# Kernel optimization log

Hardware: AMD Instinct MI355X
Metric: run time of the kernel (lower is better)

## Reference

```python
import jax, jax.numpy as jnp
import numpy as np

B, N, K = 32, 64, 128          # batch, atoms per cell, channel width (128x0e + 128x1o)
R_MAX = 5.0
NUM_BESSEL = 8
P_CUT = 5                       # num_polynomial_cutoff
AVG_NEIGH = 16.0                # avg_num_neighbors
H_MLP = 512                     # hidden_dimensions_size, n_hidden_dimensions = 2
FEAT = 5 * K                    # ((num_interactions-1)*4 + 1) * 128 = 640


def silu(x):
    return x * jax.nn.sigmoid(x)


def _bessel_cutoff(r, mask):
    # Bessel radial basis * polynomial cutoff (MACE), masked on valid edges.
    n = jnp.arange(1, NUM_BESSEL + 1, dtype=r.dtype)
    rb = jnp.sqrt(2.0 / R_MAX) * jnp.sin(n * (jnp.pi / R_MAX) * r[..., None]) / r[..., None]
    u = r / R_MAX
    p = float(P_CUT)
    fc = 1.0 - 0.5 * (p + 1) * (p + 2) * u**P_CUT + p * (p + 2) * u**(P_CUT + 1) - 0.5 * p * (p + 1) * u**(P_CUT + 2)
    fc = fc * (u < 1.0)
    return rb * (fc * mask)[..., None]


def _sph(uvec):
    # Real spherical harmonics l=0,1,2 (component normalization), uvec: unit edge vectors.
    x, y, z = uvec[..., 0], uvec[..., 1], uvec[..., 2]
    s3, s5, s15 = 3.0**0.5, 5.0**0.5, 15.0**0.5
    Y0 = jnp.ones_like(x)[..., None]
    Y1 = jnp.stack([s3 * x, s3 * y, s3 * z], -1)
    Y2 = jnp.stack([s15 * x * y, s15 * y * z, 0.5 * s5 * (3 * z * z - 1.0),
                    s15 * x * z, 0.5 * s15 * (x * x - y * y)], -1)
    return Y0, Y1, Y2


def _radial_mlp(x, w0, b0, w1, b1, w2, b2, w3, b3):
    h = silu(x @ w0 + b0)
    h = silu(h @ w1 + b1)
    h = silu(h @ w2 + b2)
    return h @ w3 + b3


def setup_inputs() -> dict:
    key = jax.random.key(0)
    ks = jax.random.split(key, 32)
    f32 = jnp.float32

    def lin(k, fan_in, shape):
        return (jax.random.normal(k, shape, dtype=f32) / np.sqrt(fan_in)).astype(f32)

    inp = {
        "noisy_relative_positions": jax.random.uniform(ks[0], (B, N, 3), dtype=f32),
        "time": jax.random.uniform(ks[1], (B, 1), dtype=f32),
        "unit_cell": (11.0 * jnp.eye(3, dtype=f32) + 0.3 * jax.random.uniform(ks[2], (B, 3, 3), dtype=f32)),
        "w_embed": lin(ks[3], 1, (K,)),
        # interaction 1 radial MLP: 8 -> 64 -> 64 -> 64 -> 3*K (weights for l=0,1,2 paths)
        "r1_w0": lin(ks[4], NUM_BESSEL, (NUM_BESSEL, 64)), "r1_b0": jnp.zeros((64,), f32),
        "r1_w1": lin(ks[5], 64, (64, 64)), "r1_b1": jnp.zeros((64,), f32),
        "r1_w2": lin(ks[6], 64, (64, 64)), "r1_b2": jnp.zeros((64,), f32),
        "r1_w3": lin(ks[7], 64, (64, 3 * K)), "r1_b3": jnp.zeros((3 * K,), f32),
        "mix1_l0": lin(ks[8], K, (K, K)),
        "mix1_l1": lin(ks[9], K, (K, K)),
        "mix1_l2": lin(ks[10], K, (K, K)),
        # interaction 2 radial MLP: 8 -> 64 -> 64 -> 64 -> 2*K (paths 0e x 0e -> 0e, 1o x 1o -> 0e)
        "r2_w0": lin(ks[11], NUM_BESSEL, (NUM_BESSEL, 64)), "r2_b0": jnp.zeros((64,), f32),
        "r2_w1": lin(ks[12], 64, (64, 64)), "r2_b1": jnp.zeros((64,), f32),
        "r2_w2": lin(ks[13], 64, (64, 64)), "r2_b2": jnp.zeros((64,), f32),
        "r2_w3": lin(ks[14], 64, (64, 2 * K)), "r2_b3": jnp.zeros((2 * K,), f32),
        "mix2": lin(ks[15], K, (K, K)),
        # readout MLP: 641 -> 512 -> 512 -> 3
        "mlp_w0": lin(ks[16], FEAT + 1, (FEAT + 1, H_MLP)), "mlp_b0": jnp.zeros((H_MLP,), f32),
        "mlp_w1": lin(ks[17], H_MLP, (H_MLP, H_MLP)), "mlp_b1": jnp.zeros((H_MLP,), f32),
        "mlp_w2": lin(ks[18], H_MLP, (H_MLP, 3)), "mlp_b2": jnp.zeros((3,), f32),
    }
    return inp


def reference(noisy_relative_positions, time, unit_cell, w_embed,
              r1_w0, r1_b0, r1_w1, r1_b1, r1_w2, r1_b2, r1_w3, r1_b3,
              mix1_l0, mix1_l1, mix1_l2,
              r2_w0, r2_b0, r2_w1, r2_b1, r2_w2, r2_b2, r2_w3, r2_b3, mix2,
              mlp_w0, mlp_b0, mlp_w1, mlp_b1, mlp_w2, mlp_b2):
    frac = noisy_relative_positions                      # [B,N,3] fractional
    d = frac[:, :, None, :] - frac[:, None, :, :]        # [B,N,N,3]
    d = d - jnp.round(d)                                 # minimum-image PBC
    dc = jnp.einsum('bijc,bcd->bijd', d, unit_cell)      # cartesian displacements
    r = jnp.sqrt(jnp.maximum(jnp.sum(dc * dc, -1), 1e-12))
    mask = (r < R_MAX) & (~jnp.eye(N, dtype=bool))[None]
    r_safe = jnp.where(mask, r, 1.0)
    uvec = dc / r_safe[..., None] * mask[..., None]      # unit edge vectors (0 off-edge)

    rad = _bessel_cutoff(r_safe, mask)                   # [B,N,N,8]
    Y0, Y1, Y2 = _sph(uvec)                              # [B,N,N,1|3|5]

    h0 = jnp.broadcast_to(w_embed, (B, N, K))            # element embedding (single species)

    # ---- interaction 1: radial-weighted tensor product h_j (x) Y_l, scatter over j ----
    we = _radial_mlp(rad, r1_w0, r1_b0, r1_w1, r1_b1, r1_w2, r1_b2, r1_w3, r1_b3)
    we = we.reshape(B, N, N, 3, K) * mask[..., None, None]
    hj = h0[:, None, :, :]                               # sender features [B,1,N,K]
    msg0 = jnp.einsum('bijk,bijm->bimk', we[..., 0, :] * hj, Y0)[:, :, 0] / AVG_NEIGH  # [B,N,K]
    msg1 = jnp.einsum('bijk,bijm->bimk', we[..., 1, :] * hj, Y1) / AVG_NEIGH           # [B,N,3,K]
    msg2 = jnp.einsum('bijk,bijm->bimk', we[..., 2, :] * hj, Y2) / AVG_NEIGH           # [B,N,5,K]

    s1 = msg0 @ mix1_l0 + jnp.sum(msg2 * msg2, axis=2) @ mix1_l2   # scalars [B,N,K]
    v1 = jnp.einsum('bimk,kc->bimc', msg1, mix1_l1)                # vectors [B,N,3,K]
    h1 = silu(s1)

    # ---- interaction 2: scalar output from 0e x 0e and 1o x 1o -> 0e paths ----
    we2 = _radial_mlp(rad, r2_w0, r2_b0, r2_w1, r2_b1, r2_w2, r2_b2, r2_w3, r2_b3)
    we2 = we2.reshape(B, N, N, 2, K) * mask[..., None, None]
    msg_a = jnp.sum(we2[..., 0, :] * h1[:, None, :, :], axis=2)    # [B,N,K]
    inv = jnp.einsum('bijm,bjmk->bijk', Y1, v1)                    # Y1 . v1_j invariant
    msg_b = jnp.sum(we2[..., 1, :] * inv, axis=2)
    s2 = ((msg_a + msg_b) / AVG_NEIGH) @ mix2                      # [B,N,K]

    # node_feats: layer1 full irreps (128x0e + 128x1o -> 512) + layer2 scalars (128) = 640
    node_feats = jnp.concatenate([s1, v1.reshape(B, N, 3 * K), s2], axis=-1)

    t = jnp.broadcast_to(time[:, None, :], (B, N, 1))
    x = jnp.concatenate([node_feats, t], axis=-1)                  # [B,N,641]
    x = jax.nn.relu(x @ mlp_w0 + mlp_b0)
    x = jax.nn.relu(x @ mlp_w1 + mlp_b1)
    return x @ mlp_w2 + mlp_b2                                     # [B,N,3]
```

## Files before the change

### kernel.cpp

```cpp
#include <hip/hip_runtime.h>
#include <math.h>

#define B_ 32
#define N_ 64
#define K_ 128
#define NPAIR (B_*N_*N_)
#define NTRI 2080
#define GEOM_BLOCKS 260
#define PREP_COUNT 741376
#define PREP_BLOCKS 2896

typedef __attribute__((ext_vector_type(8))) short short8;
typedef __attribute__((ext_vector_type(8))) __bf16 bf16x8;
typedef __attribute__((ext_vector_type(4))) float floatx4;

__device__ __forceinline__ float silu_f(float x) {
    float e = __builtin_amdgcn_exp2f(-1.442695040888963f * x);
    return x * __builtin_amdgcn_rcpf(1.0f + e);
}
__device__ __forceinline__ float4 ld4(const float* p) { return *(const float4*)p; }

__device__ __forceinline__ short f2bf(float x) {
    union { float f; unsigned u; } v; v.f = x;
    unsigned r = (v.u + 0x7FFFu + ((v.u >> 16) & 1u)) >> 16;
    return (short)r;
}
__device__ __forceinline__ float bf2f(short s) {
    union { unsigned u; float f; } v;
    v.u = ((unsigned)(unsigned short)s) << 16;
    return v.f;
}
__device__ __forceinline__ bf16x8 ld_frag(const short* p) {
    short8 r = *(const short8*)p;
    return __builtin_bit_cast(bf16x8, r);
}

__device__ __forceinline__ int2 tri_decode(int t) {
    float f = (129.0f - sqrtf((float)(16641 - 8*t))) * 0.5f;
    int i = (int)f;
    int off = 64*i - (i*(i-1))/2;
    if (off > t) { i--; off = 64*i - (i*(i-1))/2; }
    else {
        int offn = 64*(i+1) - ((i+1)*i)/2;
        if (offn <= t) { i = i+1; off = offn; }
    }
    return make_int2(i, i + (t - off));
}

__global__ __launch_bounds__(256) void pre_kernel(
    const float* __restrict__ pos, const float* __restrict__ cell,
    short* __restrict__ radbf, float* __restrict__ Y1, float* __restrict__ Y2,
    float* __restrict__ maskf,
    const float* __restrict__ r1w0, const float* __restrict__ r1w1,
    const float* __restrict__ r1w2, const float* __restrict__ r1w3,
    const float* __restrict__ r2w0, const float* __restrict__ r2w1,
    const float* __restrict__ r2w2, const float* __restrict__ r2w3,
    const float* __restrict__ r2b3,
    const float* __restrict__ mw0, const float* __restrict__ mw1,
    const float* __restrict__ wemb,
    const float* __restrict__ l0, const float* __restrict__ l1,
    const float* __restrict__ l2, short* __restrict__ dst)
{
    int t = threadIdx.x;
    if (blockIdx.x < GEOM_BLOCKS) {
        int gt = blockIdx.x * 256 + t;
        int b = gt / NTRI;
        int tt = gt - b*NTRI;
        int2 ij = tri_decode(tt);
        int i = ij.x, j = ij.y;
        const float* pi = pos + (size_t)(b*N_ + i)*3;
        const float* pj = pos + (size_t)(b*N_ + j)*3;
        float d0 = pi[0]-pj[0], d1 = pi[1]-pj[1], d2 = pi[2]-pj[2];
        d0 -= rintf(d0); d1 -= rintf(d1); d2 -= rintf(d2);
        const float* C = cell + b*9;
        float dc0 = d0*C[0] + d1*C[3] + d2*C[6];
        float dc1 = d0*C[1] + d1*C[4] + d2*C[7];
        float dc2 = d0*C[2] + d1*C[5] + d2*C[8];
        float r2 = fmaxf(dc0*dc0 + dc1*dc1 + dc2*dc2, 1e-12f);
        float r = sqrtf(r2);
        bool m = (r < 5.0f) && (i != j);
        float mf = m ? 1.0f : 0.0f;
        float rs = m ? r : 1.0f;
        float inv_rs = __builtin_amdgcn_rcpf(rs);
        inv_rs = inv_rs * (2.0f - rs*inv_rs);
        float x = dc0*inv_rs*mf, y = dc1*inv_rs*mf, z = dc2*inv_rs*mf;
        float u = r * 0.2f;
        float u2 = u*u, u4 = u2*u2, u5 = u4*u;
        float fc = 1.0f - 21.0f*u5 + 35.0f*u5*u - 15.0f*u5*u2;
        fc = (u < 1.0f) ? fc : 0.0f;
        float pref = 0.6324555320336759f * inv_rs * (fc * mf);
        float rev = 0.1f * rs;
        float sw = __builtin_amdgcn_sinf(rev);
        float cw = __builtin_amdgcn_cosf(rev);
        float c2 = 2.0f * cw;
        short8 sv;
        float sp = 0.f, s = sw;
        #pragma unroll
        for (int n = 0; n < 8; n++) {
            sv[n] = f2bf(pref * s);
            float ns = c2*s - sp;
            sp = s; s = ns;
        }
        size_t pu = ((size_t)b*64 + i)*64 + j;
        size_t pl = ((size_t)b*64 + j)*64 + i;
        *(short8*)&radbf[pu*8] = sv;
        const float s3  = 1.7320508075688772f;
        const float s5  = 2.23606797749979f;
        const float s15 = 3.872983346207417f;
        float y1x = s3*x, y1y = s3*y, y1z = s3*z;
        Y1[pu*3+0] = y1x; Y1[pu*3+1] = y1y; Y1[pu*3+2] = y1z;
        Y1[pl*3+0] = -y1x; Y1[pl*3+1] = -y1y; Y1[pl*3+2] = -y1z;
        float q0 = s15*x*y, q1 = s15*y*z, q2 = 0.5f*s5*(3.0f*z*z - 1.0f);
        float q3 = s15*x*z, q4 = 0.5f*s15*(x*x - y*y);
        Y2[pu*5+0]=q0; Y2[pu*5+1]=q1; Y2[pu*5+2]=q2; Y2[pu*5+3]=q3; Y2[pu*5+4]=q4;
        Y2[pl*5+0]=q0; Y2[pl*5+1]=q1; Y2[pl*5+2]=q2; Y2[pl*5+3]=q3; Y2[pl*5+4]=q4;
        maskf[pu] = mf; maskf[pl] = mf;
        return;
    }
    int idx = (blockIdx.x - GEOM_BLOCKS) * 256 + t;
    if (idx >= PREP_COUNT) return;
    short v;
    if (idx < 4096) {
        int n = idx >> 6, k = idx & 63; v = f2bf(r1w1[k*64 + n]);
    } else if (idx < 8192) {
        int i = idx - 4096; int n = i >> 6, k = i & 63; v = f2bf(r1w2[k*64 + n]);
    } else if (idx < 12288) {
        int i = idx - 8192; int n = i >> 6, k = i & 63; v = f2bf(r2w1[k*64 + n]);
    } else if (idx < 16384) {
        int i = idx - 12288; int n = i >> 6, k = i & 63; v = f2bf(r2w2[k*64 + n]);
    } else if (idx < 40960) {
        int i = idx - 16384; int col = i / 96, k = i - col*96;
        v = (k < 64) ? f2bf(r2w3[k*256 + col])
          : (k == 64) ? f2bf(r2b3[col]) : (short)0;
    } else if (idx < 401408) {
        int i = idx - 40960; int n = i / 704, k = i - n*704;
        v = (k < 641) ? f2bf(mw0[(size_t)k*512 + n]) : (short)0;
    } else if (idx < 663552) {
        int i = idx - 401408; int n = i >> 9, k = i & 511;
        v = f2bf(mw1[(size_t)k*512 + n]);
    } else if (idx < 665600) {
        int i = idx - 663552; int n = i >> 5, k = i & 31;
        v = (k < 8) ? f2bf(r1w0[k*64 + n]) : (short)0;
    } else if (idx < 667648) {
        int i = idx - 665600; int n = i >> 5, k = i & 31;
        v = (k < 8) ? f2bf(r2w0[k*64 + n]) : (short)0;
    } else if (idx < 692224) {
        int i = idx - 667648; int col = i >> 6, h = i & 63;
        v = f2bf(r1w3[h*384 + col] * wemb[col & 127] * 0.0625f);
    } else {
        int i = idx - 692224; int n = i / 384, k = i - n*384;
        float f;
        if (k < 128)       f = l0[k*128 + n];
        else if (k < 256)  f = l2[(k-128)*128 + n];
        else               f = l1[(k-256)*128 + n];
        v = f2bf(f);
    }
    dst[idx] = v;
}

__global__ __launch_bounds__(256) void bigmlp_kernel(
    const short* __restrict__ radbf,
    const short* __restrict__ w0T1, const float* __restrict__ b01,
    const short* __restrict__ w1T1, const float* __restrict__ b11,
    const short* __restrict__ w2T1, const float* __restrict__ b21,
    short* __restrict__ hc1,
    const short* __restrict__ w0T2, const float* __restrict__ b02,
    const short* __restrict__ w1T2, const float* __restrict__ b12,
    const short* __restrict__ w2T2, const float* __restrict__ b22,
    short* __restrict__ hc2)
{
    __shared__ short radB[128*40];
    __shared__ short actA[128*72];
    __shared__ short actB[128*72];
    __shared__ int prs[128];
    int t = threadIdx.x;
    int wv = t >> 6, lane = t & 63, qd = lane >> 4, nn = lane & 15;
    int bb = blockIdx.x / 17;
    int chunk = blockIdx.x - bb*17;

    if (t < 128) {
        int tt0 = chunk*128 + t;
        uint4 z = {0,0,0,0};
        uint4 rv = z;
        int pr = -1;
        if (tt0 < NTRI) {
            int2 ij = tri_decode(tt0);
            pr = (ij.x << 8) | ij.y;
            size_t pu = ((size_t)bb*64 + ij.x)*64 + ij.y;
            rv = *(const uint4*)&radbf[pu*8];
        }
        prs[t] = pr;
        *(uint4*)&radB[t*40]      = rv;
        *(uint4*)&radB[t*40 + 8]  = z;
        *(uint4*)&radB[t*40 + 16] = z;
        *(uint4*)&radB[t*40 + 24] = z;
        *(uint4*)&radB[t*40 + 32] = z;
    }
    __syncthreads();

    const short* w0Ts[2] = {w0T1, w0T2};
    const short* w1Ts[2] = {w1T1, w1T2};
    const short* w2Ts[2] = {w2T1, w2T2};
    const float* b0s[2]  = {b01, b02};
    const float* b1s[2]  = {b11, b12};
    const float* b2s[2]  = {b21, b22};
    short* hcs[2] = {hc1, hc2};

    for (int net = 0; net < 2; net++) {
        const short* w0T = w0Ts[net];
        const short* w1T = w1Ts[net];
        const short* w2T = w2Ts[net];
        const float* b0 = b0s[net];
        const float* b1 = b1s[net];
        const float* b2 = b2s[net];
        short* hc = hcs[net];
        #pragma unroll
        for (int ms = 0; ms < 2; ms++) {
            int r0 = wv*32 + ms*16;
            bf16x8 a = ld_frag(&radB[(r0 + nn)*40 + qd*8]);
            #pragma unroll
            for (int tt = 0; tt < 4; tt++) {
                floatx4 acc = (floatx4){0.f,0.f,0.f,0.f};
                bf16x8 bb_ = ld_frag(&w0T[(tt*16 + nn)*32 + qd*8]);
                acc = __builtin_amdgcn_mfma_f32_16x16x32_bf16(a, bb_, acc, 0, 0, 0);
                int col = tt*16 + nn;
                float bv = b0[col];
                #pragma unroll
                for (int i = 0; i < 4; i++)
                    actA[(r0 + qd*4 + i)*72 + col] = f2bf(silu_f(acc[i] + bv));
            }
        }
        __syncthreads();
        #pragma unroll
        for (int ms = 0; ms < 2; ms++) {
            int r0 = wv*32 + ms*16;
            bf16x8 a0 = ld_frag(&actA[(r0 + nn)*72 + qd*8]);
            bf16x8 a1 = ld_frag(&actA[(r0 + nn)*72 + 32 + qd*8]);
            #pragma unroll
            for (int tt = 0; tt < 4; tt++) {
                floatx4 acc = (floatx4){0.f,0.f,0.f,0.f};
                bf16x8 b0f = ld_frag(&w1T[(tt*16 + nn)*64 + qd*8]);
                bf16x8 b1f = ld_frag(&w1T[(tt*16 + nn)*64 + 32 + qd*8]);
                acc = __builtin_amdgcn_mfma_f32_16x16x32_bf16(a0, b0f, acc, 0, 0, 0);
                acc = __builtin_amdgcn_mfma_f32_16x16x32_bf16(a1, b1f, acc, 0, 0, 0);
                int col = tt*16 + nn;
                float bv = b1[col];
                #pragma unroll
                for (int i = 0; i < 4; i++)
                    actB[(r0 + qd*4 + i)*72 + col] = f2bf(silu_f(acc[i] + bv));
            }
        }
        __syncthreads();
        #pragma unroll
        for (int ms = 0; ms < 2; ms++) {
            int r0 = wv*32 + ms*16;
            bf16x8 a0 = ld_frag(&actB[(r0 + nn)*72 + qd*8]);
            bf16x8 a1 = ld_frag(&actB[(r0 + nn)*72 + 32 + qd*8]);
            #pragma unroll
            for (int tt = 0; tt < 4; tt++) {
                floatx4 acc = (floatx4){0.f,0.f,0.f,0.f};
                bf16x8 b0f = ld_frag(&w2T[(tt*16 + nn)*64 + qd*8]);
                bf16x8 b1f = ld_frag(&w2T[(tt*16 + nn)*64 + 32 + qd*8]);
                acc = __builtin_amdgcn_mfma_f32_16x16x32_bf16(a0, b0f, acc, 0, 0, 0);
                acc = __builtin_amdgcn_mfma_f32_16x16x32_bf16(a1, b1f, acc, 0, 0, 0);
                int col = tt*16 + nn;
                float bv = b2[col];
                #pragma unroll
                for (int i = 0; i < 4; i++) {
                    int pr = prs[r0 + qd*4 + i];
                    if (pr >= 0) {
                        short val = f2bf(silu_f(acc[i] + bv));
                        int pi = pr >> 8, pj = pr & 255;
                        size_t base = (size_t)bb*4096;
                        hc[(base + pi*64 + pj)*64 + col] = val;
                        if (pi != pj)
                            hc[(base + pj*64 + pi)*64 + col] = val;
                    }
                }
            }
        }
        __syncthreads();
    }
}

__global__ __launch_bounds__(256) void msg1_kernel(
    const short* __restrict__ hc1, const float* __restrict__ Y1g,
    const float* __restrict__ Y2g, const float* __restrict__ maskg,
    const float* __restrict__ wemb, const float* __restrict__ b3,
    const short* __restrict__ w3T, const short* __restrict__ lT,
    const float* __restrict__ timeg,
    short* __restrict__ h1bf, float* __restrict__ v1g, short* __restrict__ featsb)
{
    __shared__ __align__(16) char pool[19008];
    short* hcT  = (short*)pool;
    short* A2   = (short*)pool;
    short* YmB  = (short*)(pool + 9216);
    short* GB   = (short*)(pool + 11520);
    float* msgF = (float*)(pool + 13824);
    float* qF   = (float*)(pool + 18432);
    float* SY   = (float*)(pool + 18944);

    int t = threadIdx.x;
    int wv = t >> 6, lane = t & 63, qd = lane >> 4, nn = lane & 15;
    int node = blockIdx.x;
    int b = node >> 6;
    size_t pbase = (size_t)node * 64;

    for (int idx = t; idx < 512; idx += 256) {
        int j = idx >> 3, h0 = (idx & 7)*8;
        short8 v = *(const short8*)&hc1[((size_t)node*64 + j)*64 + h0];
        #pragma unroll
        for (int q = 0; q < 8; q++) hcT[(h0 + q)*72 + j] = v[q];
    }
    for (int idx = t; idx < 1152; idx += 256) YmB[idx] = 0;
    __syncthreads();
    if (t < 64) {
        int j = t;
        float mf = maskg[pbase + j];
        YmB[j] = f2bf(mf);
        #pragma unroll
        for (int m = 0; m < 3; m++) YmB[(1+m)*72 + j] = f2bf(Y1g[(pbase+j)*3 + m] * mf);
        #pragma unroll
        for (int m = 0; m < 5; m++) YmB[(4+m)*72 + j] = f2bf(Y2g[(pbase+j)*5 + m] * mf);
    }
    __syncthreads();
    if (t < 16) {
        float acc = 0.f;
        if (t < 9) for (int j = 0; j < 64; j++) acc += bf2f(YmB[t*72 + j]);
        SY[t] = acc;
    }
    {
        floatx4 accG = (floatx4){0.f,0.f,0.f,0.f};
        #pragma unroll
        for (int ks = 0; ks < 64; ks += 32) {
            bf16x8 a = ld_frag(&YmB[nn*72 + ks + qd*8]);
            bf16x8 bfr = ld_frag(&hcT[(wv*16 + nn)*72 + ks + qd*8]);
            accG = __builtin_amdgcn_mfma_f32_16x16x32_bf16(a, bfr, accG, 0, 0, 0);
        }
        #pragma unroll
        for (int i = 0; i < 4; i++)
            GB[(qd*4 + i)*72 + wv*16 + nn] = f2bf(accG[i]);
    }
    __syncthreads();
    {
        bf16x8 a0f = ld_frag(&GB[nn*72 + 0  + qd*8]);
        bf16x8 a1f = ld_frag(&GB[nn*72 + 32 + qd*8]);
        #pragma unroll
        for (int tl = 0; tl < 6; tl++) {
            int col0 = (wv*6 + tl)*16;
            floatx4 acc = (floatx4){0.f,0.f,0.f,0.f};
            bf16x8 b0f = ld_frag(&w3T[(col0 + nn)*64 + 0  + qd*8]);
            bf16x8 b1f = ld_frag(&w3T[(col0 + nn)*64 + 32 + qd*8]);
            acc = __builtin_amdgcn_mfma_f32_16x16x32_bf16(a0f, b0f, acc, 0, 0, 0);
            acc = __builtin_amdgcn_mfma_f32_16x16x32_bf16(a1f, b1f, acc, 0, 0, 0);
            int col = col0 + nn;
            int csec = col >> 7, k = col & 127;
            #pragma unroll
            for (int i = 0; i < 4; i++) {
                int m = qd*4 + i;
                bool valid = (csec == 0) ? (m == 0)
                           : (csec == 1) ? (m >= 1 && m <= 3)
                                         : (m >= 4 && m <= 8);
                if (valid)
                    msgF[m*128 + k] = acc[i] + SY[m]*b3[col]*wemb[k]*0.0625f;
            }
        }
    }
    __syncthreads();
    if (t < 128) {
        float acc = 0.f;
        #pragma unroll
        for (int m = 4; m < 9; m++) { float v = msgF[m*128 + t]; acc += v*v; }
        qF[t] = acc;
    }
    __syncthreads();
    for (int idx = t; idx < 6272; idx += 256) A2[idx] = 0;
    __syncthreads();
    A2[t] = (t < 128) ? f2bf(msgF[t]) : f2bf(qF[t - 128]);
    if (t < 128) {
        #pragma unroll
        for (int m = 1; m <= 3; m++)
            A2[m*392 + 256 + t] = f2bf(msgF[m*128 + t]);
    }
    __syncthreads();
    #pragma unroll
    for (int tt = 0; tt < 2; tt++) {
        int col = (wv*2 + tt)*16 + nn;
        floatx4 acc = (floatx4){0.f,0.f,0.f,0.f};
        #pragma unroll
        for (int ks = 0; ks < 384; ks += 32) {
            bf16x8 a = ld_frag(&A2[nn*392 + ks + qd*8]);
            bf16x8 bfr = ld_frag(&lT[(size_t)col*384 + ks + qd*8]);
            acc = __builtin_amdgcn_mfma_f32_16x16x32_bf16(a, bfr, acc, 0, 0, 0);
        }
        if (qd == 0) {
            float s1 = acc[0];
            featsb[(size_t)node*704 + col] = f2bf(s1);
            h1bf[(size_t)node*128 + col] = f2bf(silu_f(s1));
            #pragma unroll
            for (int i = 1; i < 4; i++) {
                float v = acc[i];
                v1g[(size_t)node*384 + (i-1)*128 + col] = v;
                featsb[(size_t)node*704 + 128 + (i-1)*128 + col] = f2bf(v);
            }
        }
    }
    if (t == 0) featsb[(size_t)node*704 + 640] = f2bf(timeg[b]);
    if (t < 63) featsb[(size_t)node*704 + 641 + t] = 0;
}

__global__ __launch_bounds__(256) void msg2_kernel(
    const short* __restrict__ hc2, const float* __restrict__ Y1g,
    const float* __restrict__ maskg, const short* __restrict__ w3extT,
    const short* __restrict__ h1bf, const float* __restrict__ v1g,
    const float* __restrict__ mix2, short* __restrict__ featsb)
{
    __shared__ __align__(16) char pool[50688];
    short* hc2e  = (short*)pool;
    short* h1B   = (short*)(pool + 14336);
    short* invB  = (short*)(pool + 31744);
    float* Y1s   = (float*)(pool + 49152);
    float* msgab = (float*)(pool + 50176);

    int t = threadIdx.x;
    int wv = t >> 6, lane = t & 63, qd = lane >> 4, nn = lane & 15;
    int node = blockIdx.x;
    int b = node >> 6;
    size_t pbase = (size_t)node * 64;

    if (t < 64) {
        int j = t;
        #pragma unroll
        for (int m = 0; m < 3; m++) Y1s[j*4 + m] = Y1g[(pbase+j)*3 + m];
        float mf = maskg[pbase + j];
        short8 z8 = {0,0,0,0,0,0,0,0};
        *(short8*)&hc2e[j*112 + 64] = z8;
        *(short8*)&hc2e[j*112 + 72] = z8;
        *(short8*)&hc2e[j*112 + 80] = z8;
        *(short8*)&hc2e[j*112 + 88] = z8;
        *(short8*)&hc2e[j*112 + 96] = z8;
        *(short8*)&hc2e[j*112 + 104] = z8;
        hc2e[j*112 + 64] = f2bf(mf);
    }
    for (int idx = t; idx < 512; idx += 256) {
        int j = idx >> 3, h0 = (idx & 7)*8;
        short8 v = *(const short8*)&hc2[((size_t)node*64 + j)*64 + h0];
        float mf = maskg[pbase + j];
        if (mf == 0.f) { short8 z8 = {0,0,0,0,0,0,0,0}; v = z8; }
        *(short8*)&hc2e[j*112 + h0] = v;
    }
    for (int idx = t; idx < 1024; idx += 256) {
        int j = idx >> 4, k0 = (idx & 15)*8;
        *(uint4*)&h1B[j*136 + k0] = *(const uint4*)&h1bf[((size_t)b*64 + j)*128 + k0];
    }
    if (t < 128) msgab[t] = 0.f;
    __syncthreads();
    for (int idx = t; idx < 2048; idx += 256) {
        int j = idx >> 5, kq = (idx & 31)*4;
        const float* vb = &v1g[((size_t)b*64 + j)*384 + kq];
        float4 vx = ld4(vb), vy = ld4(vb + 128), vz = ld4(vb + 256);
        float yx = Y1s[j*4+0], yy = Y1s[j*4+1], yz = Y1s[j*4+2];
        invB[j*136 + kq + 0] = f2bf(yx*vx.x + yy*vy.x + yz*vz.x);
        invB[j*136 + kq + 1] = f2bf(yx*vx.y + yy*vy.y + yz*vz.y);
        invB[j*136 + kq + 2] = f2bf(yx*vx.z + yy*vy.z + yz*vz.z);
        invB[j*136 + kq + 3] = f2bf(yx*vx.w + yy*vy.w + yz*vz.w);
    }
    __syncthreads();
    {
        bf16x8 a0 = ld_frag(&hc2e[(wv*16 + nn)*112 + 0  + qd*8]);
        bf16x8 a1 = ld_frag(&hc2e[(wv*16 + nn)*112 + 32 + qd*8]);
        bf16x8 a2 = ld_frag(&hc2e[(wv*16 + nn)*112 + 64 + qd*8]);
        for (int g = 0; g < 4; g++) {
            #pragma unroll
            for (int tt = 0; tt < 4; tt++) {
                int col0 = g*64 + tt*16;
                floatx4 acc = (floatx4){0.f,0.f,0.f,0.f};
                bf16x8 b0f = ld_frag(&w3extT[(col0 + nn)*96 + 0  + qd*8]);
                bf16x8 b1f = ld_frag(&w3extT[(col0 + nn)*96 + 32 + qd*8]);
                bf16x8 b2f = ld_frag(&w3extT[(col0 + nn)*96 + 64 + qd*8]);
                acc = __builtin_amdgcn_mfma_f32_16x16x32_bf16(a0, b0f, acc, 0, 0, 0);
                acc = __builtin_amdgcn_mfma_f32_16x16x32_bf16(a1, b1f, acc, 0, 0, 0);
                acc = __builtin_amdgcn_mfma_f32_16x16x32_bf16(a2, b2f, acc, 0, 0, 0);
                int col = col0 + nn;
                int k = col & 127;
                const short* src = (col < 128) ? h1B : invB;
                float p = 0.f;
                #pragma unroll
                for (int i = 0; i < 4; i++) {
                    int j = wv*16 + qd*4 + i;
                    p += acc[i] * bf2f(src[j*136 + k]);
                }
                p += __shfl_xor(p, 16);
                p += __shfl_xor(p, 32);
                if (qd == 0) atomicAdd(&msgab[k], p);
            }
        }
    }
    __syncthreads();
    if (t < 128) {
        float acc = 0.f;
        for (int k = 0; k < 128; k++) acc += msgab[k] * mix2[k*128 + t];
        featsb[(size_t)node*704 + 512 + t] = f2bf(acc * 0.0625f);
    }
}

__global__ __launch_bounds__(256) void gemm_part_kernel(
    const short* __restrict__ A, int lda,
    const short* __restrict__ BT, int ldb,
    int ngran, int nsplit, float* __restrict__ Cp)
{
    int t = threadIdx.x;
    int wv = t >> 6, lane = t & 63, qd = lane >> 4, nn = lane & 15;
    int m0 = blockIdx.x * 64, n0 = blockIdx.y * 64, z = blockIdx.z;
    int g0 = (z*ngran)/nsplit, g1 = ((z+1)*ngran)/nsplit;
    floatx4 acc[4];
    #pragma unroll
    for (int tt = 0; tt < 4; tt++) acc[tt] = (floatx4){0.f,0.f,0.f,0.f};
    int row = wv*16 + nn;
    for (int g = g0; g < g1; g++) {
        int k = g*32;
        bf16x8 a = ld_frag(&A[(size_t)(m0 + row)*lda + k + qd*8]);
        #pragma unroll
        for (int tt = 0; tt < 4; tt++) {
            bf16x8 bb = ld_frag(&BT[(size_t)(n0 + tt*16 + nn)*ldb + k + qd*8]);
            acc[tt] = __builtin_amdgcn_mfma_f32_16x16x32_bf16(a, bb, acc[tt], 0, 0, 0);
        }
    }
    float* out = Cp + (size_t)z*2048*512;
    #pragma unroll
    for (int tt = 0; tt < 4; tt++) {
        int n = n0 + tt*16 + nn;
        #pragma unroll
        for (int i = 0; i < 4; i++)
            out[(size_t)(m0 + wv*16 + qd*4 + i)*512 + n] = acc[tt][i];
    }
}

__global__ __launch_bounds__(256) void combine_kernel(
    const float* __restrict__ Cp, const float* __restrict__ bias,
    short* __restrict__ out)
{
    int idx = (blockIdx.x * 256 + threadIdx.x) * 4;
    int n = idx & 511;
    float4 s = ld4(&Cp[idx]);
    #pragma unroll
    for (int z = 1; z < 4; z++) {
        float4 p = ld4(&Cp[(size_t)z*1048576 + idx]);
        s.x += p.x; s.y += p.y; s.z += p.z; s.w += p.w;
    }
    float4 bv = ld4(&bias[n]);
    short4 o;
    o.x = f2bf(fmaxf(s.x + bv.x, 0.f));
    o.y = f2bf(fmaxf(s.y + bv.y, 0.f));
    o.z = f2bf(fmaxf(s.z + bv.z, 0.f));
    o.w = f2bf(fmaxf(s.w + bv.w, 0.f));
    *(short4*)&out[idx] = o;
}

__global__ __launch_bounds__(64) void final3_kernel(
    const short* __restrict__ H, const float* __restrict__ w2,
    const float* __restrict__ b2, float* __restrict__ out)
{
    int node = blockIdx.x, lane = threadIdx.x;
    float a0 = 0.f, a1 = 0.f, a2 = 0.f;
    #pragma unroll
    for (int r = 0; r < 8; r++) {
        int k = r*64 + lane;
        float h = bf2f(H[(size_t)node*512 + k]);
        a0 += h * w2[k*3 + 0];
        a1 += h * w2[k*3 + 1];
        a2 += h * w2[k*3 + 2];
    }
    #pragma unroll
    for (int off = 32; off > 0; off >>= 1) {
        a0 += __shfl_down(a0, off);
        a1 += __shfl_down(a1, off);
        a2 += __shfl_down(a2, off);
    }
    if (lane == 0) {
        out[(size_t)node*3 + 0] = a0 + b2[0];
        out[(size_t)node*3 + 1] = a1 + b2[1];
        out[(size_t)node*3 + 2] = a2 + b2[2];
    }
}

extern "C" void kernel_launch(void* const* d_in, const int* in_sizes, int n_in,
                              void* d_out, int out_size, void* d_ws, size_t ws_size,
                              hipStream_t stream) {
    const float* pos   = (const float*)d_in[0];
    const float* timeg = (const float*)d_in[1];
    const float* cell  = (const float*)d_in[2];
    const float* wemb  = (const float*)d_in[3];
    const float* r1w0  = (const float*)d_in[4];
    const float* r1b0  = (const float*)d_in[5];
    const float* r1w1  = (const float*)d_in[6];
    const float* r1b1  = (const float*)d_in[7];
    const float* r1w2  = (const float*)d_in[8];
    const float* r1b2  = (const float*)d_in[9];
    const float* r1w3  = (const float*)d_in[10];
    const float* r1b3  = (const float*)d_in[11];
    const float* l0    = (const float*)d_in[12];
    const float* l1    = (const float*)d_in[13];
    const float* l2    = (const float*)d_in[14];
    const float* r2w0  = (const float*)d_in[15];
    const float* r2b0  = (const float*)d_in[16];
    const float* r2w1  = (const float*)d_in[17];
    const float* r2b1  = (const float*)d_in[18];
    const float* r2w2  = (const float*)d_in[19];
    const float* r2b2  = (const float*)d_in[20];
    const float* r2w3  = (const float*)d_in[21];
    const float* r2b3  = (const float*)d_in[22];
    const float* mix2  = (const float*)d_in[23];
    const float* mw0   = (const float*)d_in[24];
    const float* mb0   = (const float*)d_in[25];
    const float* mw1   = (const float*)d_in[26];
    const float* mb1   = (const float*)d_in[27];
    const float* mw2   = (const float*)d_in[28];
    const float* mb2   = (const float*)d_in[29];

    float* ws = (float*)d_ws;
    short* radbf  = (short*)ws;
    float* Y1     = ws + 524288;
    float* Y2     = ws + 917504;
    float* maskf  = ws + 1572864;
    float* v1     = ws + 1703936;
    short* featsb = (short*)(ws + 2490368);
    short* prep   = (short*)(ws + 3211264);
    short* hc1    = (short*)(ws + 3590144);
    short* hc2    = (short*)(ws + 7784448);
    short* h1bf   = (short*)(ws + 11978752);

    short* w1T_1  = prep;
    short* w2T_1  = prep + 4096;
    short* w1T_2  = prep + 8192;
    short* w2T_2  = prep + 12288;
    short* w3extT = prep + 16384;
    short* wT0    = prep + 40960;
    short* wT1    = prep + 401408;
    short* w0T_1  = prep + 663552;
    short* w0T_2  = prep + 665600;
    short* w3T_1  = prep + 667648;
    short* lT     = prep + 692224;

    float* Cp   = (float*)hc1;
    short* h0bb = radbf;
    short* h1bb = (short*)Y2;

    pre_kernel<<<GEOM_BLOCKS + PREP_BLOCKS, 256, 0, stream>>>(
        pos, cell, radbf, Y1, Y2, maskf,
        r1w0, r1w1, r1w2, r1w3, r2w0, r2w1, r2w2, r2w3, r2b3,
        mw0, mw1, wemb, l0, l1, l2, prep);
    bigmlp_kernel<<<32*17, 256, 0, stream>>>(radbf,
        w0T_1, r1b0, w1T_1, r1b1, w2T_1, r1b2, hc1,
        w0T_2, r2b0, w1T_2, r2b1, w2T_2, r2b2, hc2);
    msg1_kernel<<<B_*N_, 256, 0, stream>>>(hc1, Y1, Y2, maskf, wemb, r1b3,
        w3T_1, lT, timeg, h1bf, v1, featsb);
    msg2_kernel<<<B_*N_, 256, 0, stream>>>(hc2, Y1, maskf, w3extT, h1bf, v1,
        mix2, featsb);
    {
        dim3 g(32, 8, 4);
        gemm_part_kernel<<<g, 256, 0, stream>>>(featsb, 704, wT0, 704, 22, 4, Cp);
        combine_kernel<<<1024, 256, 0, stream>>>(Cp, mb0, h0bb);
        gemm_part_kernel<<<g, 256, 0, stream>>>(h0bb, 512, wT1, 512, 16, 4, Cp);
        combine_kernel<<<1024, 256, 0, stream>>>(Cp, mb1, h1bb);
    }
    final3_kernel<<<B_*N_, 64, 0, stream>>>(h1bb, mw2, mb2, (float*)d_out);
}
```

Before: 301.2 us.

## Restructure msg2 into two-node blocks, fold mask into MLP, fuse final combine

The mask is now applied inside the radial MLP epilogue, so msg2 no longer needs the extended bias/mask column and the w3 operand shrinks to K=64 with the bias added after the MFMA. msg2 becomes msg2b, which handles two nodes per block with double-buffered Y1/mask staging, loads hc2 fragments straight from global memory, and replaces shared atomics with per-wave partial sums. The last combine kernel is folded into the final 3-output projection, which now reads the fp32 split-K partials directly. The zero-fill passes in msg1 are also trimmed to only the padding regions, removing two barriers. Risks: reading the fp32 partials in the final kernel costs more bandwidth than bf16, and fewer, larger msg2 blocks reduce parallelism.

```diff
diff --git a/kernel.cpp b/kernel.cpp
--- a/kernel.cpp
+++ b/kernel.cpp
@@ -9,6 +9,7 @@
 #define GEOM_BLOCKS 260
 #define PREP_COUNT 741376
 #define PREP_BLOCKS 2896
+#define NPB 2
 
 typedef __attribute__((ext_vector_type(8))) short short8;
 typedef __attribute__((ext_vector_type(8))) __bf16 bf16x8;
@@ -55,7 +56,6 @@
     const float* __restrict__ r1w2, const float* __restrict__ r1w3,
     const float* __restrict__ r2w0, const float* __restrict__ r2w1,
     const float* __restrict__ r2w2, const float* __restrict__ r2w3,
-    const float* __restrict__ r2b3,
     const float* __restrict__ mw0, const float* __restrict__ mw1,
     const float* __restrict__ wemb,
     const float* __restrict__ l0, const float* __restrict__ l1,
@@ -129,9 +129,8 @@
     } else if (idx < 16384) {
         int i = idx - 12288; int n = i >> 6, k = i & 63; v = f2bf(r2w2[k*64 + n]);
     } else if (idx < 40960) {
-        int i = idx - 16384; int col = i / 96, k = i - col*96;
-        v = (k < 64) ? f2bf(r2w3[k*256 + col])
-          : (k == 64) ? f2bf(r2b3[col]) : (short)0;
+        int i = idx - 16384;
+        v = (i < 16384) ? f2bf(r2w3[(i & 63)*256 + (i >> 6)]) : (short)0;
     } else if (idx < 401408) {
         int i = idx - 40960; int n = i / 704, k = i - n*704;
         v = (k < 641) ? f2bf(mw0[(size_t)k*512 + n]) : (short)0;
@@ -159,7 +158,7 @@
 }
 
 __global__ __launch_bounds__(256) void bigmlp_kernel(
-    const short* __restrict__ radbf,
+    const short* __restrict__ radbf, const float* __restrict__ maskg,
     const short* __restrict__ w0T1, const float* __restrict__ b01,
     const short* __restrict__ w1T1, const float* __restrict__ b11,
     const short* __restrict__ w2T1, const float* __restrict__ b21,
@@ -173,6 +172,7 @@
     __shared__ short actA[128*72];
     __shared__ short actB[128*72];
     __shared__ int prs[128];
+    __shared__ float maskv[128];
     int t = threadIdx.x;
     int wv = t >> 6, lane = t & 63, qd = lane >> 4, nn = lane & 15;
     int bb = blockIdx.x / 17;
@@ -183,13 +183,16 @@
         uint4 z = {0,0,0,0};
         uint4 rv = z;
         int pr = -1;
+        float mv = 0.f;
         if (tt0 < NTRI) {
             int2 ij = tri_decode(tt0);
             pr = (ij.x << 8) | ij.y;
             size_t pu = ((size_t)bb*64 + ij.x)*64 + ij.y;
             rv = *(const uint4*)&radbf[pu*8];
+            mv = maskg[pu];
         }
         prs[t] = pr;
+        maskv[t] = mv;
         *(uint4*)&radB[t*40]      = rv;
         *(uint4*)&radB[t*40 + 8]  = z;
         *(uint4*)&radB[t*40 + 16] = z;
@@ -267,9 +270,10 @@
                 float bv = b2[col];
                 #pragma unroll
                 for (int i = 0; i < 4; i++) {
-                    int pr = prs[r0 + qd*4 + i];
+                    int ridx = r0 + qd*4 + i;
+                    int pr = prs[ridx];
                     if (pr >= 0) {
-                        short val = f2bf(silu_f(acc[i] + bv));
+                        short val = f2bf(silu_f(acc[i] + bv) * maskv[ridx]);
                         int pi = pr >> 8, pj = pr & 255;
                         size_t base = (size_t)bb*4096;
                         hc[(base + pi*64 + pj)*64 + col] = val;
@@ -312,8 +316,7 @@
         #pragma unroll
         for (int q = 0; q < 8; q++) hcT[(h0 + q)*72 + j] = v[q];
     }
-    for (int idx = t; idx < 1152; idx += 256) YmB[idx] = 0;
-    __syncthreads();
+    for (int idx = t; idx < 504; idx += 256) YmB[648 + idx] = 0;
     if (t < 64) {
         int j = t;
         float mf = maskg[pbase + j];
@@ -343,6 +346,8 @@
     }
     __syncthreads();
     {
+        short8 z8 = {0,0,0,0,0,0,0,0};
+        for (int idx = t; idx < 720; idx += 256) *(short8*)&A2[idx*8] = z8;
         bf16x8 a0f = ld_frag(&GB[nn*72 + 0  + qd*8]);
         bf16x8 a1f = ld_frag(&GB[nn*72 + 32 + qd*8]);
         #pragma unroll
@@ -367,14 +372,14 @@
         }
     }
     __syncthreads();
+    A2[5760 + t] = 0;
+    A2[6016 + t] = 0;
     if (t < 128) {
         float acc = 0.f;
         #pragma unroll
         for (int m = 4; m < 9; m++) { float v = msgF[m*128 + t]; acc += v*v; }
         qF[t] = acc;
     }
-    __syncthreads();
-    for (int idx = t; idx < 6272; idx += 256) A2[idx] = 0;
     __syncthreads();
     A2[t] = (t < 128) ? f2bf(msgF[t]) : f2bf(qF[t - 128]);
     if (t < 128) {
@@ -409,98 +414,112 @@
     if (t < 63) featsb[(size_t)node*704 + 641 + t] = 0;
 }
 
-__global__ __launch_bounds__(256) void msg2_kernel(
+__global__ __launch_bounds__(256) void msg2b_kernel(
     const short* __restrict__ hc2, const float* __restrict__ Y1g,
-    const float* __restrict__ maskg, const short* __restrict__ w3extT,
-    const short* __restrict__ h1bf, const float* __restrict__ v1g,
-    const float* __restrict__ mix2, short* __restrict__ featsb)
+    const float* __restrict__ maskg, const short* __restrict__ w3T2,
+    const float* __restrict__ b3, const short* __restrict__ h1bf,
+    const float* __restrict__ v1g, const float* __restrict__ mix2,
+    short* __restrict__ featsb)
 {
-    __shared__ __align__(16) char pool[50688];
-    short* hc2e  = (short*)pool;
-    short* h1B   = (short*)(pool + 14336);
-    short* invB  = (short*)(pool + 31744);
-    float* Y1s   = (float*)(pool + 49152);
-    float* msgab = (float*)(pool + 50176);
+    __shared__ __align__(16) char pool[39424];
+    short* srcH = (short*)pool;
+    short* srcI = (short*)(pool + 17408);
+    float* msgW = (float*)(pool + 34816);
+    float* y1m  = (float*)(pool + 36864);
+    float* mrow = (float*)(pool + 36864 + 2048);
 
     int t = threadIdx.x;
     int wv = t >> 6, lane = t & 63, qd = lane >> 4, nn = lane & 15;
-    int node = blockIdx.x;
-    int b = node >> 6;
-    size_t pbase = (size_t)node * 64;
+    int b = blockIdx.x >> 5;
+    int ig = blockIdx.x & 31;
+    int i0 = ig * NPB;
 
     if (t < 64) {
         int j = t;
-        #pragma unroll
-        for (int m = 0; m < 3; m++) Y1s[j*4 + m] = Y1g[(pbase+j)*3 + m];
-        float mf = maskg[pbase + j];
-        short8 z8 = {0,0,0,0,0,0,0,0};
-        *(short8*)&hc2e[j*112 + 64] = z8;
-        *(short8*)&hc2e[j*112 + 72] = z8;
-        *(short8*)&hc2e[j*112 + 80] = z8;
-        *(short8*)&hc2e[j*112 + 88] = z8;
-        *(short8*)&hc2e[j*112 + 96] = z8;
-        *(short8*)&hc2e[j*112 + 104] = z8;
-        hc2e[j*112 + 64] = f2bf(mf);
-    }
-    for (int idx = t; idx < 512; idx += 256) {
-        int j = idx >> 3, h0 = (idx & 7)*8;
-        short8 v = *(const short8*)&hc2[((size_t)node*64 + j)*64 + h0];
-        float mf = maskg[pbase + j];
-        if (mf == 0.f) { short8 z8 = {0,0,0,0,0,0,0,0}; v = z8; }
-        *(short8*)&hc2e[j*112 + h0] = v;
-    }
-    for (int idx = t; idx < 1024; idx += 256) {
-        int j = idx >> 4, k0 = (idx & 15)*8;
-        *(uint4*)&h1B[j*136 + k0] = *(const uint4*)&h1bf[((size_t)b*64 + j)*128 + k0];
-    }
-    if (t < 128) msgab[t] = 0.f;
+        size_t pb = ((size_t)(b*64 + i0))*64 + j;
+        float mf = maskg[pb];
+        mrow[j] = mf;
+        #pragma unroll
+        for (int m = 0; m < 3; m++) y1m[j*4 + m] = Y1g[pb*3 + m] * mf;
+    }
     __syncthreads();
-    for (int idx = t; idx < 2048; idx += 256) {
-        int j = idx >> 5, kq = (idx & 31)*4;
-        const float* vb = &v1g[((size_t)b*64 + j)*384 + kq];
-        float4 vx = ld4(vb), vy = ld4(vb + 128), vz = ld4(vb + 256);
-        float yx = Y1s[j*4+0], yy = Y1s[j*4+1], yz = Y1s[j*4+2];
-        invB[j*136 + kq + 0] = f2bf(yx*vx.x + yy*vy.x + yz*vz.x);
-        invB[j*136 + kq + 1] = f2bf(yx*vx.y + yy*vy.y + yz*vz.y);
-        invB[j*136 + kq + 2] = f2bf(yx*vx.z + yy*vy.z + yz*vz.z);
-        invB[j*136 + kq + 3] = f2bf(yx*vx.w + yy*vy.w + yz*vz.w);
-    }
-    __syncthreads();
-    {
-        bf16x8 a0 = ld_frag(&hc2e[(wv*16 + nn)*112 + 0  + qd*8]);
-        bf16x8 a1 = ld_frag(&hc2e[(wv*16 + nn)*112 + 32 + qd*8]);
-        bf16x8 a2 = ld_frag(&hc2e[(wv*16 + nn)*112 + 64 + qd*8]);
-        for (int g = 0; g < 4; g++) {
+
+    for (int ii = 0; ii < NPB; ii++) {
+        int i = i0 + ii;
+        size_t node = (size_t)b*64 + i;
+        int cur = ii & 1;
+        const float* y1c = y1m + cur*256;
+        const float* mrc = mrow + cur*64;
+
+        for (int idx = t; idx < 2048; idx += 256) {
+            int j = idx >> 5, kq = (idx & 31)*4;
+            uint2 hv = *(const uint2*)&h1bf[((size_t)b*64 + j)*128 + kq];
+            if (mrc[j] == 0.f) { hv.x = 0u; hv.y = 0u; }
+            *(uint2*)&srcH[j*136 + kq] = hv;
+            const float* vb = &v1g[((size_t)b*64 + j)*384 + kq];
+            float4 vx = ld4(vb), vy = ld4(vb + 128), vz = ld4(vb + 256);
+            float yx = y1c[j*4], yy = y1c[j*4+1], yz = y1c[j*4+2];
+            srcI[j*136 + kq + 0] = f2bf(yx*vx.x + yy*vy.x + yz*vz.x);
+            srcI[j*136 + kq + 1] = f2bf(yx*vx.y + yy*vy.y + yz*vz.y);
+            srcI[j*136 + kq + 2] = f2bf(yx*vx.z + yy*vy.z + yz*vz.z);
+            srcI[j*136 + kq + 3] = f2bf(yx*vx.w + yy*vy.w + yz*vz.w);
+        }
+        __syncthreads();
+
+        {
+            const short* arow = &hc2[(node*64 + (size_t)(wv*16 + nn))*64];
+            bf16x8 a0 = ld_frag(arow + qd*8);
+            bf16x8 a1 = ld_frag(arow + 32 + qd*8);
             #pragma unroll
-            for (int tt = 0; tt < 4; tt++) {
-                int col0 = g*64 + tt*16;
-                floatx4 acc = (floatx4){0.f,0.f,0.f,0.f};
-                bf16x8 b0f = ld_frag(&w3extT[(col0 + nn)*96 + 0  + qd*8]);
-                bf16x8 b1f = ld_frag(&w3extT[(col0 + nn)*96 + 32 + qd*8]);
-                bf16x8 b2f = ld_frag(&w3extT[(col0 + nn)*96 + 64 + qd*8]);
-                acc = __builtin_amdgcn_mfma_f32_16x16x32_bf16(a0, b0f, acc, 0, 0, 0);
-                acc = __builtin_amdgcn_mfma_f32_16x16x32_bf16(a1, b1f, acc, 0, 0, 0);
-                acc = __builtin_amdgcn_mfma_f32_16x16x32_bf16(a2, b2f, acc, 0, 0, 0);
-                int col = col0 + nn;
-                int k = col & 127;
-                const short* src = (col < 128) ? h1B : invB;
+            for (int tt = 0; tt < 8; tt++) {
+                int col0 = tt*16 + nn;
+                int col1 = col0 + 128;
+                floatx4 acc0 = (floatx4){0.f,0.f,0.f,0.f};
+                floatx4 acc1 = (floatx4){0.f,0.f,0.f,0.f};
+                bf16x8 b00 = ld_frag(&w3T2[(size_t)col0*64 + qd*8]);
+                bf16x8 b01 = ld_frag(&w3T2[(size_t)col0*64 + 32 + qd*8]);
+                bf16x8 b10 = ld_frag(&w3T2[(size_t)col1*64 + qd*8]);
+                bf16x8 b11 = ld_frag(&w3T2[(size_t)col1*64 + 32 + qd*8]);
+                acc0 = __builtin_amdgcn_mfma_f32_16x16x32_bf16(a0, b00, acc0, 0, 0, 0);
+                acc0 = __builtin_amdgcn_mfma_f32_16x16x32_bf16(a1, b01, acc0, 0, 0, 0);
+                acc1 = __builtin_amdgcn_mfma_f32_16x16x32_bf16(a0, b10, acc1, 0, 0, 0);
+                acc1 = __builtin_amdgcn_mfma_f32_16x16x32_bf16(a1, b11, acc1, 0, 0, 0);
+                float bb0 = b3[col0], bb1 = b3[col1];
                 float p = 0.f;
                 #pragma unroll
-                for (int i = 0; i < 4; i++) {
-                    int j = wv*16 + qd*4 + i;
-                    p += acc[i] * bf2f(src[j*136 + k]);
+                for (int i4 = 0; i4 < 4; i4++) {
+                    int j = wv*16 + qd*4 + i4;
+                    p += (acc0[i4] + bb0) * bf2f(srcH[j*136 + col0])
+                       + (acc1[i4] + bb1) * bf2f(srcI[j*136 + col0]);
                 }
                 p += __shfl_xor(p, 16);
                 p += __shfl_xor(p, 32);
-                if (qd == 0) atomicAdd(&msgab[k], p);
+                if (qd == 0) msgW[wv*128 + col0] = p;
             }
         }
-    }
-    __syncthreads();
-    if (t < 128) {
-        float acc = 0.f;
-        for (int k = 0; k < 128; k++) acc += msgab[k] * mix2[k*128 + t];
-        featsb[(size_t)node*704 + 512 + t] = f2bf(acc * 0.0625f);
+        __syncthreads();
+
+        if (t < 128) {
+            msgW[t] = msgW[t] + msgW[128 + t] + msgW[256 + t] + msgW[384 + t];
+        } else if (ii + 1 < NPB) {
+            int j = t - 128;
+            if (j < 64) {
+                size_t pb = ((size_t)(b*64 + i0 + ii + 1))*64 + j;
+                float mf = maskg[pb];
+                int nx = (ii + 1) & 1;
+                mrow[nx*64 + j] = mf;
+                #pragma unroll
+                for (int m = 0; m < 3; m++)
+                    y1m[nx*256 + j*4 + m] = Y1g[pb*3 + m] * mf;
+            }
+        }
+        __syncthreads();
+
+        if (t < 128) {
+            float acc = 0.f;
+            for (int k = 0; k < 128; k++) acc += msgW[k] * mix2[k*128 + t];
+            featsb[node*704 + 512 + t] = f2bf(acc * 0.0625f);
+        }
     }
 }
 
@@ -557,16 +576,20 @@
     *(short4*)&out[idx] = o;
 }
 
-__global__ __launch_bounds__(64) void final3_kernel(
-    const short* __restrict__ H, const float* __restrict__ w2,
-    const float* __restrict__ b2, float* __restrict__ out)
+__global__ __launch_bounds__(64) void final3b_kernel(
+    const float* __restrict__ Cp, const float* __restrict__ b1,
+    const float* __restrict__ w2, const float* __restrict__ b2,
+    float* __restrict__ out)
 {
     int node = blockIdx.x, lane = threadIdx.x;
     float a0 = 0.f, a1 = 0.f, a2 = 0.f;
     #pragma unroll
     for (int r = 0; r < 8; r++) {
         int k = r*64 + lane;
-        float h = bf2f(H[(size_t)node*512 + k]);
+        size_t off = (size_t)node*512 + k;
+        float h = Cp[off] + Cp[1048576 + off] + Cp[2*1048576 + off]
+                + Cp[3*1048576 + off] + b1[k];
+        h = fmaxf(h, 0.f);
         a0 += h * w2[k*3 + 0];
         a1 += h * w2[k*3 + 1];
         a2 += h * w2[k*3 + 2];
@@ -634,7 +657,7 @@
     short* w2T_1  = prep + 4096;
     short* w1T_2  = prep + 8192;
     short* w2T_2  = prep + 12288;
-    short* w3extT = prep + 16384;
+    short* w3T2   = prep + 16384;
     short* wT0    = prep + 40960;
     short* wT1    = prep + 401408;
     short* w0T_1  = prep + 663552;
@@ -644,25 +667,23 @@
 
     float* Cp   = (float*)hc1;
     short* h0bb = radbf;
-    short* h1bb = (short*)Y2;
 
     pre_kernel<<<GEOM_BLOCKS + PREP_BLOCKS, 256, 0, stream>>>(
         pos, cell, radbf, Y1, Y2, maskf,
-        r1w0, r1w1, r1w2, r1w3, r2w0, r2w1, r2w2, r2w3, r2b3,
+        r1w0, r1w1, r1w2, r1w3, r2w0, r2w1, r2w2, r2w3,
         mw0, mw1, wemb, l0, l1, l2, prep);
-    bigmlp_kernel<<<32*17, 256, 0, stream>>>(radbf,
+    bigmlp_kernel<<<32*17, 256, 0, stream>>>(radbf, maskf,
         w0T_1, r1b0, w1T_1, r1b1, w2T_1, r1b2, hc1,
         w0T_2, r2b0, w1T_2, r2b1, w2T_2, r2b2, hc2);
     msg1_kernel<<<B_*N_, 256, 0, stream>>>(hc1, Y1, Y2, maskf, wemb, r1b3,
         w3T_1, lT, timeg, h1bf, v1, featsb);
-    msg2_kernel<<<B_*N_, 256, 0, stream>>>(hc2, Y1, maskf, w3extT, h1bf, v1,
-        mix2, featsb);
+    msg2b_kernel<<<32*32, 256, 0, stream>>>(hc2, Y1, maskf, w3T2, r2b3,
+        h1bf, v1, mix2, featsb);
     {
         dim3 g(32, 8, 4);
         gemm_part_kernel<<<g, 256, 0, stream>>>(featsb, 704, wT0, 704, 22, 4, Cp);
         combine_kernel<<<1024, 256, 0, stream>>>(Cp, mb0, h0bb);
         gemm_part_kernel<<<g, 256, 0, stream>>>(h0bb, 512, wT1, 512, 16, 4, Cp);
-        combine_kernel<<<1024, 256, 0, stream>>>(Cp, mb1, h1bb);
-    }
-    final3_kernel<<<B_*N_, 64, 0, stream>>>(h1bb, mw2, mb2, (float*)d_out);
-}
+    }
+    final3b_kernel<<<B_*N_, 64, 0, stream>>>(Cp, mb1, mw2, mb2, (float*)d_out);
+}
```

After: 287.4 us. 4.6% less time.
